# Performance work log

Measured on AMD Instinct MI355X. Metric: run time of the kernel, lower is better.

The kernel has to match this reference:

```python
import jax, jax.numpy as jnp
import numpy as np

WINDOW = 256   # init kwarg window_size
CAUSAL = False # init kwarg causal


def setup_inputs() -> dict:
    key = jax.random.key(0)
    k1, k2, k3 = jax.random.split(key, 3)
    shape = (2, 16, 4096, 64)  # (batch, heads, seq_len, head_dim); seq_len % WINDOW == 0
    return {
        "query": jax.random.normal(k1, shape, dtype=jnp.float32),
        "key": jax.random.normal(k2, shape, dtype=jnp.float32),
        "value": jax.random.normal(k3, shape, dtype=jnp.float32),
    }


def _neighbor_blocks(x, nb, W):
    # x: [B,H,S,D] -> [B,H,nb,3W,D] where block n holds key blocks n-1,n,n+1 (zero padded at ends)
    B, H, S, D = x.shape
    xb = x.reshape(B, H, nb, W, D)
    xp = jnp.pad(xb, ((0, 0), (0, 0), (1, 1), (0, 0), (0, 0)))
    return jnp.concatenate([xp[:, :, j:j + nb] for j in range(3)], axis=3)


def _swa(query, key, value, window, causal):
    B, H, S, D = query.shape
    W = window
    nb = S // W
    scale = jnp.float32(1.0 / np.sqrt(D))
    qb = query.reshape(B, H, nb, W, D)
    kb = _neighbor_blocks(key, nb, W)    # [B,H,nb,3W,D]
    vb = _neighbor_blocks(value, nb, W)  # [B,H,nb,3W,D]

    # band mask: query global pos qi = n*W + q, key global pos ki = n*W + (k - W)
    qpos = jnp.arange(W)[:, None]              # [W,1]
    kpos = jnp.arange(3 * W)[None, :] - W      # [1,3W] relative block offset
    diff = kpos - qpos                         # [W,3W] == ki - qi
    ki = jnp.arange(nb)[:, None, None] * W + kpos[None]  # [nb,1,3W]
    valid = (ki >= 0) & (ki < S)
    if causal:
        band = (diff >= -W) & (diff <= 0)
    else:
        band = jnp.abs(diff) <= W
    mask = valid & band[None]                  # [nb,W,3W]

    scores = jnp.einsum('bhnqd,bhnkd->bhnqk', qb, kb) * scale  # [B,H,nb,W,3W]
    scores = jnp.where(mask, scores, -jnp.inf)
    attn = jax.nn.softmax(scores, axis=-1)
    out = jnp.einsum('bhnqk,bhnkd->bhnqd', attn, vb)
    return out.reshape(B, H, S, D)


def reference(query, key, value):
    return _swa(query, key, value, WINDOW, CAUSAL)
```

## Files before the change

### kernel.cpp

```cpp
#include <hip/hip_runtime.h>
#include <hip/hip_bf16.h>

typedef __attribute__((ext_vector_type(4)))  float f32x4;
typedef __attribute__((ext_vector_type(16))) float f32x16;
typedef __attribute__((ext_vector_type(8)))  short bf16x8;
typedef __attribute__((ext_vector_type(4)))  unsigned u32x4;

#define S_LEN 4096
#define HEAD_D 64
#define WIN 256
#define QBLK 128
#define KVBLK 64
#define KSTR 72
#define VSTR 72
#define QSCALE 0.18033688f

#define KBYTES (KVBLK * KSTR * 2)
#define VBYTES (HEAD_D * VSTR * 2)
#define KHALF  (KBYTES / 2)
#define VHALF  (VBYTES / 2)
#define LPAR_OFF (2 * KBYTES + 2 * VBYTES)
#define SMEM_BYTES (LPAR_OFF + 2 * 4 * 32 * 4)

static __device__ __forceinline__ unsigned cvt2(float lo, float hi) {
  unsigned r;
  asm("v_cvt_pk_bf16_f32 %0, %1, %2" : "=v"(r) : "v"(lo), "v"(hi));
  return r;
}

#define PUB_BARRIER() do {                              \
    __builtin_amdgcn_sched_barrier(0);                  \
    asm volatile("s_waitcnt lgkmcnt(0)" ::: "memory");  \
    __builtin_amdgcn_s_barrier();                       \
    __builtin_amdgcn_sched_barrier(0);                  \
  } while (0)

__global__ __launch_bounds__(512, 4)
void swa_fwd(const float* __restrict__ Q, const float* __restrict__ K,
             const float* __restrict__ V, float* __restrict__ O) {
  __shared__ __attribute__((aligned(16))) char smem[SMEM_BYTES];

  const int tid  = threadIdx.x;
  const int widx = tid >> 6;
  const int lane = tid & 63;
  const int hi   = lane >> 5;
  const int c    = lane & 31;
  const int qg   = widx & 3;
  const int kh   = widx >> 2;
  const int kho  = kh * 32;

  const int pb  = blockIdx.x;
  const int bh  = (pb & 7) * 4 + ((pb >> 3) >> 5);
  const int qb  = (pb >> 3) & 31;
  const int bq0 = qb * QBLK;
  const int q0w = bq0 + qg * 32;

  const size_t base = (size_t)bh * S_LEN * HEAD_D;
  const float* Qp = Q + base;
  const float* Kp = K + base;
  const float* Vp = V + base;
  float*       Op = O + base;

  const f32x16 Z16 = {0.f,0.f,0.f,0.f,0.f,0.f,0.f,0.f,0.f,0.f,0.f,0.f,0.f,0.f,0.f,0.f};

  bf16x8 aq[4];
  {
    const float* qr = Qp + (size_t)(q0w + c) * HEAD_D + hi * 8;
    #pragma unroll
    for (int ch = 0; ch < 4; ++ch) {
      f32x4 x0 = *(const f32x4*)(qr + ch * 16);
      f32x4 x1 = *(const f32x4*)(qr + ch * 16 + 4);
      u32x4 au;
      au[0] = cvt2(x0[0] * QSCALE, x0[1] * QSCALE);
      au[1] = cvt2(x0[2] * QSCALE, x0[3] * QSCALE);
      au[2] = cvt2(x1[0] * QSCALE, x1[1] * QSCALE);
      au[3] = cvt2(x1[2] * QSCALE, x1[3] * QSCALE);
      aq[ch] = __builtin_bit_cast(bf16x8, au);
    }
  }

  f32x16 acc0 = Z16, acc1 = Z16;
  float lsA = 0.f, lsB = 0.f;

  const int lo   = max(0, bq0 - WIN);
  const int khiB = min(S_LEN, bq0 + QBLK + WIN);
  const int nt   = (khiB - lo) >> 6;

  const int krow  = tid >> 3;
  const int kc8   = (tid & 7) << 3;
  const int key2  = (tid & 31) << 1;
  const int key2p = (key2 & ~12) | ((key2 & 4) << 1) | ((key2 & 8) >> 1);
  const int vd4   = (tid >> 5) << 2;

  short* const ksh = (short*)smem;
  short* const vsh = (short*)(smem + 2 * KBYTES);
  const short* const krd = ksh + (kho + c) * KSTR + hi * 8;
  const short* const vrd = vsh + c * VSTR + kho + hi * 8;
  short* const kwr = ksh + krow * KSTR + kc8;
  short* const vwr = vsh + vd4 * VSTR + key2p;

  unsigned koff = (unsigned)(lo + krow) * HEAD_D + kc8;
  unsigned voff = (unsigned)(lo + key2) * HEAD_D + vd4;

  f32x4 ka0, ka1, va0, va1;
  #define LOAD_TILE() do {                          \
    ka0 = *(const f32x4*)(Kp + koff);               \
    ka1 = *(const f32x4*)(Kp + koff + 4);           \
    va0 = *(const f32x4*)(Vp + voff);               \
    va1 = *(const f32x4*)(Vp + voff + HEAD_D);      \
    koff += KVBLK * HEAD_D;                         \
    voff += KVBLK * HEAD_D;                         \
  } while (0)

  #define STAGE_TO(BUF) do {                                        \
    u32x4 kw;                                                       \
    kw[0] = cvt2(ka0[0], ka0[1]);                                   \
    kw[1] = cvt2(ka0[2], ka0[3]);                                   \
    kw[2] = cvt2(ka1[0], ka1[1]);                                   \
    kw[3] = cvt2(ka1[2], ka1[3]);                                   \
    *(u32x4*)&kwr[(BUF) * KHALF] = kw;                              \
    _Pragma("unroll")                                               \
    for (int j = 0; j < 4; ++j)                                     \
      *(unsigned*)&vwr[(BUF) * VHALF + j * VSTR] = cvt2(va0[j], va1[j]); \
  } while (0)

  #define TILE_BODY(T, BUF) do {                                              \
    const int rel_ = lo + ((T) << 6) + kho - q0w;                             \
    const bool live_ = (rel_ >= -287) && (rel_ <= 287);                       \
    f32x16 s = Z16;                                                           \
    if (live_) {                                                              \
      __builtin_amdgcn_s_setprio(1);                                          \
      _Pragma("unroll")                                                       \
      for (int ch = 0; ch < 4; ++ch) {                                        \
        bf16x8 akf = *(const bf16x8*)&krd[(BUF) * KHALF + ch * 16];           \
        s = __builtin_amdgcn_mfma_f32_32x32x16_bf16(akf, aq[ch], s, 0, 0, 0); \
      }                                                                       \
      __builtin_amdgcn_s_setprio(0);                                          \
    }                                                                         \
    if ((T) + 1 < nt) {                                                       \
      STAGE_TO((BUF) ^ 1);                                                    \
      if ((T) + 2 < nt) LOAD_TILE();                                          \
    }                                                                         \
    if (live_) {                                                              \
      if (rel_ >= -224 && rel_ <= 224) {                                      \
        _Pragma("unroll")                                                     \
        for (int g = 0; g < 16; g += 2) {                                     \
          const float p0 = __builtin_amdgcn_exp2f(s[g]);                      \
          const float p1 = __builtin_amdgcn_exp2f(s[g + 1]);                  \
          s[g] = p0; s[g + 1] = p1; lsA += p0; lsB += p1;                     \
        }                                                                     \
      } else {                                                                \
        const int bm_ = rel_ + 4 * hi - c + WIN;                              \
        _Pragma("unroll")                                                     \
        for (int g = 0; g < 16; ++g) {                                        \
          const int ro_ = (g & 3) + 8 * (g >> 2);                             \
          const float p = ((unsigned)(bm_ + ro_) <= 2u * WIN)                 \
                            ? __builtin_amdgcn_exp2f(s[g]) : 0.f;             \
          s[g] = p; if (g & 1) lsB += p; else lsA += p;                       \
        }                                                                     \
      }                                                                       \
      __builtin_amdgcn_s_setprio(1);                                          \
      _Pragma("unroll")                                                       \
      for (int kt = 0; kt < 2; ++kt) {                                        \
        u32x4 pau;                                                            \
        _Pragma("unroll")                                                     \
        for (int p2 = 0; p2 < 4; ++p2)                                        \
          pau[p2] = cvt2(s[kt * 8 + 2 * p2], s[kt * 8 + 2 * p2 + 1]);         \
        const bf16x8 pa = __builtin_bit_cast(bf16x8, pau);                    \
        bf16x8 bv0 = *(const bf16x8*)&vrd[(BUF) * VHALF + kt * 16];           \
        acc0 = __builtin_amdgcn_mfma_f32_32x32x16_bf16(pa, bv0, acc0, 0,0,0); \
        bf16x8 bv1 = *(const bf16x8*)&vrd[(BUF) * VHALF + kt * 16 + 32 * VSTR]; \
        acc1 = __builtin_amdgcn_mfma_f32_32x32x16_bf16(pa, bv1, acc1, 0,0,0); \
      }                                                                       \
      __builtin_amdgcn_s_setprio(0);                                          \
    }                                                                         \
    if ((T) + 1 < nt) PUB_BARRIER();                                          \
  } while (0)

  LOAD_TILE();
  STAGE_TO(0);
  LOAD_TILE();
  PUB_BARRIER();

  for (int t = 0; t < nt; t += 2) {
    TILE_BODY(t, 0);
    TILE_BODY(t + 1, 1);
  }

  float lsum = lsA + lsB;
  lsum += __shfl_xor(lsum, 32);
  __syncthreads();
  float* o_mrg = (float*)smem;
  float* l_par = (float*)(smem + LPAR_OFF);
  if (hi == 0) l_par[(kh * 4 + qg) * 32 + c] = lsum;
  if (kh == 0) {
    #pragma unroll
    for (int g = 0; g < 16; ++g) {
      const int qrow = (g & 3) + 8 * (g >> 2) + 4 * hi;
      o_mrg[(qg * 32 + qrow) * HEAD_D + c]      = acc0[g];
      o_mrg[(qg * 32 + qrow) * HEAD_D + 32 + c] = acc1[g];
    }
  }
  __syncthreads();
  if (kh == 1) {
    if (hi == 0) l_par[qg * 32 + c] = 1.0f / (l_par[qg * 32 + c] + l_par[(4 + qg) * 32 + c]);
    __asm__ volatile("s_waitcnt lgkmcnt(0)" ::: "memory");
    __builtin_amdgcn_sched_barrier(0);
    #pragma unroll
    for (int g = 0; g < 16; ++g) {
      const int qrow = (g & 3) + 8 * (g >> 2) + 4 * hi;
      const float iv = l_par[qg * 32 + qrow];
      float* orow = Op + (size_t)(q0w + qrow) * HEAD_D;
      orow[c]      = (o_mrg[(qg * 32 + qrow) * HEAD_D + c]      + acc0[g]) * iv;
      orow[32 + c] = (o_mrg[(qg * 32 + qrow) * HEAD_D + 32 + c] + acc1[g]) * iv;
    }
  }
}

extern "C" void kernel_launch(void* const* d_in, const int* in_sizes, int n_in,
                              void* d_out, int out_size, void* d_ws, size_t ws_size,
                              hipStream_t stream) {
  const float* q = (const float*)d_in[0];
  const float* k = (const float*)d_in[1];
  const float* v = (const float*)d_in[2];
  float* o = (float*)d_out;
  const int blocks = 2 * 16 * (S_LEN / QBLK);
  swa_fwd<<<dim3(blocks), dim3(512), 0, stream>>>(q, k, v, o);
}
```

Baseline: 47.03 us.

## Software-pipeline PV MFMA one tile behind QK with quad-buffered V

Restructures the KV loop so each tile's P·V MFMAs are issued during the next tile's QK MFMA step. The softmax probabilities are packed and carried across the barrier, and V gets four shared-memory buffers so the previous tile's V stays valid while the next one is staged. The goal is to overlap matrix work with the exp and conversion work and hide latency within each wave. The cost is more LDS and registers, and launch bounds drop from 4 to 2 blocks per CU, which lowers occupancy.

```diff
diff --git a/kernel.cpp b/kernel.cpp
--- a/kernel.cpp
+++ b/kernel.cpp
@@ -15,11 +15,11 @@
 #define VSTR 72
 #define QSCALE 0.18033688f
 
-#define KBYTES (KVBLK * KSTR * 2)
-#define VBYTES (HEAD_D * VSTR * 2)
-#define KHALF  (KBYTES / 2)
-#define VHALF  (VBYTES / 2)
-#define LPAR_OFF (2 * KBYTES + 2 * VBYTES)
+#define KELEM (KVBLK * KSTR)
+#define VELEM (HEAD_D * VSTR)
+#define KBYTES (KELEM * 2)
+#define VOFF   (2 * KBYTES)
+#define LPAR_OFF (VOFF + 4 * KBYTES)
 #define SMEM_BYTES (LPAR_OFF + 2 * 4 * 32 * 4)
 
 static __device__ __forceinline__ unsigned cvt2(float lo, float hi) {
@@ -35,7 +35,7 @@
     __builtin_amdgcn_sched_barrier(0);                  \
   } while (0)
 
-__global__ __launch_bounds__(512, 4)
+__global__ __launch_bounds__(512, 2)
 void swa_fwd(const float* __restrict__ Q, const float* __restrict__ K,
              const float* __restrict__ V, float* __restrict__ O) {
   __shared__ __attribute__((aligned(16))) char smem[SMEM_BYTES];
@@ -93,7 +93,7 @@
   const int vd4   = (tid >> 5) << 2;
 
   short* const ksh = (short*)smem;
-  short* const vsh = (short*)(smem + 2 * KBYTES);
+  short* const vsh = (short*)(smem + VOFF);
   const short* const krd = ksh + (kho + c) * KSTR + hi * 8;
   const short* const vrd = vsh + c * VSTR + kho + hi * 8;
   short* const kwr = ksh + krow * KSTR + kc8;
@@ -112,34 +112,53 @@
     voff += KVBLK * HEAD_D;                         \
   } while (0)
 
-  #define STAGE_TO(BUF) do {                                        \
+  #define STAGE_TO(KB, VB) do {                                     \
     u32x4 kw;                                                       \
     kw[0] = cvt2(ka0[0], ka0[1]);                                   \
     kw[1] = cvt2(ka0[2], ka0[3]);                                   \
     kw[2] = cvt2(ka1[0], ka1[1]);                                   \
     kw[3] = cvt2(ka1[2], ka1[3]);                                   \
-    *(u32x4*)&kwr[(BUF) * KHALF] = kw;                              \
+    *(u32x4*)&kwr[(KB) * KELEM] = kw;                               \
     _Pragma("unroll")                                               \
     for (int j = 0; j < 4; ++j)                                     \
-      *(unsigned*)&vwr[(BUF) * VHALF + j * VSTR] = cvt2(va0[j], va1[j]); \
-  } while (0)
-
-  #define TILE_BODY(T, BUF) do {                                              \
-    const int rel_ = lo + ((T) << 6) + kho - q0w;                             \
+      *(unsigned*)&vwr[(VB) * VELEM + j * VSTR] = cvt2(va0[j], va1[j]); \
+  } while (0)
+
+  u32x4 paAp, paBp;
+  bool  livp = false;
+
+  #define DO_PV(VBP) do {                                                     \
+    __builtin_amdgcn_s_setprio(1);                                            \
+    const bf16x8 pa0 = __builtin_bit_cast(bf16x8, paAp);                      \
+    bf16x8 bv00 = *(const bf16x8*)&vrd[(VBP) * VELEM];                        \
+    acc0 = __builtin_amdgcn_mfma_f32_32x32x16_bf16(pa0, bv00, acc0, 0, 0, 0); \
+    bf16x8 bv01 = *(const bf16x8*)&vrd[(VBP) * VELEM + 32 * VSTR];            \
+    acc1 = __builtin_amdgcn_mfma_f32_32x32x16_bf16(pa0, bv01, acc1, 0, 0, 0); \
+    const bf16x8 pa1 = __builtin_bit_cast(bf16x8, paBp);                      \
+    bf16x8 bv10 = *(const bf16x8*)&vrd[(VBP) * VELEM + 16];                   \
+    acc0 = __builtin_amdgcn_mfma_f32_32x32x16_bf16(pa1, bv10, acc0, 0, 0, 0); \
+    bf16x8 bv11 = *(const bf16x8*)&vrd[(VBP) * VELEM + 16 + 32 * VSTR];       \
+    acc1 = __builtin_amdgcn_mfma_f32_32x32x16_bf16(pa1, bv11, acc1, 0, 0, 0); \
+    __builtin_amdgcn_s_setprio(0);                                            \
+  } while (0)
+
+  #define INTERVAL(N, KB, VBNXT, VBPREV) do {                                 \
+    const int rel_ = lo + ((N) << 6) + kho - q0w;                             \
     const bool live_ = (rel_ >= -287) && (rel_ <= 287);                       \
     f32x16 s = Z16;                                                           \
     if (live_) {                                                              \
       __builtin_amdgcn_s_setprio(1);                                          \
       _Pragma("unroll")                                                       \
       for (int ch = 0; ch < 4; ++ch) {                                        \
-        bf16x8 akf = *(const bf16x8*)&krd[(BUF) * KHALF + ch * 16];           \
+        bf16x8 akf = *(const bf16x8*)&krd[(KB) * KELEM + ch * 16];            \
         s = __builtin_amdgcn_mfma_f32_32x32x16_bf16(akf, aq[ch], s, 0, 0, 0); \
       }                                                                       \
       __builtin_amdgcn_s_setprio(0);                                          \
     }                                                                         \
-    if ((T) + 1 < nt) {                                                       \
-      STAGE_TO((BUF) ^ 1);                                                    \
-      if ((T) + 2 < nt) LOAD_TILE();                                          \
+    if (livp) DO_PV(VBPREV);                  \
+    if ((N) + 1 < nt) {                                                       \
+      STAGE_TO((KB) ^ 1, VBNXT);                                              \
+      if ((N) + 2 < nt) LOAD_TILE();                                          \
     }                                                                         \
     if (live_) {                                                              \
       if (rel_ >= -224 && rel_ <= 224) {                                      \
@@ -159,32 +178,35 @@
           s[g] = p; if (g & 1) lsB += p; else lsA += p;                       \
         }                                                                     \
       }                                                                       \
-      __builtin_amdgcn_s_setprio(1);                                          \
       _Pragma("unroll")                                                       \
-      for (int kt = 0; kt < 2; ++kt) {                                        \
-        u32x4 pau;                                                            \
-        _Pragma("unroll")                                                     \
-        for (int p2 = 0; p2 < 4; ++p2)                                        \
-          pau[p2] = cvt2(s[kt * 8 + 2 * p2], s[kt * 8 + 2 * p2 + 1]);         \
-        const bf16x8 pa = __builtin_bit_cast(bf16x8, pau);                    \
-        bf16x8 bv0 = *(const bf16x8*)&vrd[(BUF) * VHALF + kt * 16];           \
-        acc0 = __builtin_amdgcn_mfma_f32_32x32x16_bf16(pa, bv0, acc0, 0,0,0); \
-        bf16x8 bv1 = *(const bf16x8*)&vrd[(BUF) * VHALF + kt * 16 + 32 * VSTR]; \
-        acc1 = __builtin_amdgcn_mfma_f32_32x32x16_bf16(pa, bv1, acc1, 0,0,0); \
+      for (int p2 = 0; p2 < 4; ++p2) {                                        \
+        paAp[p2] = cvt2(s[2 * p2], s[2 * p2 + 1]);                            \
+        paBp[p2] = cvt2(s[8 + 2 * p2], s[8 + 2 * p2 + 1]);                    \
       }                                                                       \
-      __builtin_amdgcn_s_setprio(0);                                          \
     }                                                                         \
-    if ((T) + 1 < nt) PUB_BARRIER();                                          \
+    livp = live_;                                                             \
+    if ((N) + 1 < nt) PUB_BARRIER();                                          \
   } while (0)
 
   LOAD_TILE();
-  STAGE_TO(0);
+  STAGE_TO(0, 0);
   LOAD_TILE();
   PUB_BARRIER();
 
-  for (int t = 0; t < nt; t += 2) {
-    TILE_BODY(t, 0);
-    TILE_BODY(t + 1, 1);
+  int n = 0;
+  for (; n + 4 <= nt; n += 4) {
+    INTERVAL(n + 0, 0, 1, 3);
+    INTERVAL(n + 1, 1, 2, 0);
+    INTERVAL(n + 2, 0, 3, 1);
+    INTERVAL(n + 3, 1, 0, 2);
+  }
+  if (nt & 2) {
+    INTERVAL(n + 0, 0, 1, 3);
+    INTERVAL(n + 1, 1, 2, 0);
+  }
+  if (livp) {
+    if (((nt - 1) & 3) == 1) DO_PV(1);
+    else                     DO_PV(3);
   }
 
   float lsum = lsA + lsB;
```

After: 54.38 us. 15.6% more time.
